# Performance work log

Hardware: AMD Instinct MI355X
Metric: run time of the kernel (lower is better)

The kernel has to match this reference:

```python
import jax, jax.numpy as jnp
import numpy as np

D_MODEL = 1024
N_HEADS = 16
HEAD_DIM = D_MODEL // N_HEADS
EPS = 1e-6


def _phi(x):
    # elu(x) + 1 feature map
    return jax.nn.elu(x) + 1.0


def setup_inputs() -> dict:
    key = jax.random.key(0)
    ks = jax.random.split(key, 12)
    B, N, M = 4, 4096, 4096
    s = 1.0 / np.sqrt(D_MODEL)
    return {
        "queries": jax.random.normal(ks[0], (B, N, D_MODEL), jnp.float32),
        "keys": jax.random.normal(ks[1], (B, M, D_MODEL), jnp.float32),
        "values": jax.random.normal(ks[2], (B, M, D_MODEL), jnp.float32),
        "wq": jax.random.normal(ks[3], (D_MODEL, D_MODEL), jnp.float32) * s,
        "bq": jax.random.normal(ks[4], (D_MODEL,), jnp.float32) * s,
        "wk": jax.random.normal(ks[5], (D_MODEL, D_MODEL), jnp.float32) * s,
        "bk": jax.random.normal(ks[6], (D_MODEL,), jnp.float32) * s,
        "wv": jax.random.normal(ks[7], (D_MODEL, D_MODEL), jnp.float32) * s,
        "bv": jax.random.normal(ks[8], (D_MODEL,), jnp.float32) * s,
        "wo": jax.random.normal(ks[9], (D_MODEL, D_MODEL), jnp.float32) * s,
        "bo": jax.random.normal(ks[10], (D_MODEL,), jnp.float32) * s,
    }


def reference(queries, keys, values, wq, bq, wk, bk, wv, bv, wo, bo):
    B, N, _ = queries.shape
    M = keys.shape[1]
    H, Dh = N_HEADS, HEAD_DIM
    # projections + head split -> [B, H, seq, Dh]
    q = _phi((queries @ wq.T + bq).reshape(B, N, H, Dh).transpose(0, 2, 1, 3))
    k = _phi((keys @ wk.T + bk).reshape(B, M, H, Dh).transpose(0, 2, 1, 3))
    v = (values @ wv.T + bv).reshape(B, M, H, Dh).transpose(0, 2, 1, 3)
    # kv aggregation: [B,H,Dh,Dh]
    kv = jnp.einsum("bhmd,bhme->bhde", k, v)
    # normalizer: [B,H,Dh]
    z = k.sum(axis=2)
    num = jnp.einsum("bhnd,bhde->bhne", q, kv)
    den = jnp.einsum("bhnd,bhd->bhn", q, z)[..., None] + EPS
    out = (num / den).transpose(0, 2, 1, 3).reshape(B, N, H * Dh)
    return out @ wo.T + bo
```

## Files before the change

kernel.cpp:

```cpp
#include <hip/hip_runtime.h>

#define EPS 1e-6f

typedef __attribute__((ext_vector_type(8))) __bf16 bf16x8;
typedef __attribute__((ext_vector_type(4))) float f32x4;
typedef __attribute__((ext_vector_type(4))) unsigned short us4v;
typedef __attribute__((ext_vector_type(8))) unsigned short us8v;
typedef unsigned short us;

__device__ inline us f2bf(float f) {
  unsigned int u = __builtin_bit_cast(unsigned int, f);
  unsigned int r = (u + 0x7fffu + ((u >> 16) & 1u)) >> 16;
  return (us)r;
}
__device__ inline float bf2f(us s) {
  unsigned int u = ((unsigned int)s) << 16;
  return __builtin_bit_cast(float, u);
}
__device__ inline unsigned int cvtpk(float a, float b) {
  unsigned int d;
  asm("v_cvt_pk_bf16_f32 %0, %1, %2" : "=v"(d) : "v"(a), "v"(b));
  return d;
}

__device__ inline void gl_lds16(const us* g, us* l) {
  __builtin_amdgcn_global_load_lds(
      (const __attribute__((address_space(1))) unsigned int*)g,
      (__attribute__((address_space(3))) unsigned int*)l, 16, 0, 0);
}

__global__ __launch_bounds__(256) void conv_w4(const float* __restrict__ wq,
                                               const float* __restrict__ wk,
                                               const float* __restrict__ wv,
                                               const float* __restrict__ wo,
                                               us* __restrict__ dq,
                                               us* __restrict__ dk,
                                               us* __restrict__ dv,
                                               us* __restrict__ dwo) {
  int bid = blockIdx.x;
  int msel = bid >> 9, lb = bid & 511;
  const float* s = (msel == 0) ? wq : (msel == 1) ? wk : (msel == 2) ? wv : wo;
  us* d = (msel == 0) ? dq : (msel == 1) ? dk : (msel == 2) ? dv : dwo;
  int idx = lb * 256 + threadIdx.x;
  size_t base = (size_t)idx * 8;
  float4 a = *(const float4*)(s + base);
  float4 b = *(const float4*)(s + base + 4);
  us8v o;
  o[0] = f2bf(a.x); o[1] = f2bf(a.y); o[2] = f2bf(a.z); o[3] = f2bf(a.w);
  o[4] = f2bf(b.x); o[5] = f2bf(b.y); o[6] = f2bf(b.z); o[7] = f2bf(b.w);
  *(us8v*)(d + base) = o;
}

template <int MODE>
__global__ __launch_bounds__(512, 2) void proj_gemm(const void* __restrict__ Xv,
                                                    const us* __restrict__ W,
                                                    const float* __restrict__ bias,
                                                    void* __restrict__ Yv) {
  constexpr bool FP32X = (MODE != 3);
  __shared__ alignas(16) us As[2][256 * 64];
  __shared__ alignas(16) us Bs[2][256 * 64];

  const float* Xf = (const float*)Xv;
  const us* Xh = (const us*)Xv;

  const int t = threadIdx.x;
  const int wave = t >> 6, lane = t & 63;
  const int q4 = lane >> 4, l16 = lane & 15;
  const int wm = wave >> 2, wn = wave & 3;
  const int bid = blockIdx.x;
  const int rowg = (bid & 7) * 8 + (bid >> 5);
  const int colg = (bid >> 3) & 3;
  const int rowBase = rowg << 8;
  const int colBase = colg << 8;

  const int tr = t >> 3;
  const int g8 = ((t & 7) ^ (tr & 7)) * 8;
  const us* Wg = W + (size_t)(colBase + tr) * 1024 + g8;

  const int gx0 = ((0 | q4) ^ (l16 & 7)) * 8;
  const int gx1 = ((4 | q4) ^ (l16 & 7)) * 8;
  const int arow_off = (wm * 128 + l16) * 64;
  const int brow_off = (wn * 64 + l16) * 64;

  float4 av[2][2][2];
  uint4 aw[2][2];

  f32x4 acc[8][4];
#pragma unroll
  for (int i = 0; i < 8; i++)
#pragma unroll
    for (int j = 0; j < 4; j++) acc[i][j] = (f32x4){0.f, 0.f, 0.f, 0.f};

#define ISSUE_A(kt, h)                                                       \
  if constexpr (FP32X) {                                                     \
    const float* p_ = Xf + (size_t)(rowBase + (h) * 128 + tr) * 1024 +       \
                      (kt) * 64 + g8;                                        \
    av[h][0][0] = *(const float4*)p_;                                        \
    av[h][0][1] = *(const float4*)(p_ + 4);                                  \
    av[h][1][0] = *(const float4*)(p_ + 65536);                              \
    av[h][1][1] = *(const float4*)(p_ + 65536 + 4);                          \
  } else {                                                                   \
    const us* p_ = Xh + (size_t)(rowBase + (h) * 128 + tr) * 1024 +          \
                   (kt) * 64 + g8;                                           \
    aw[h][0] = *(const uint4*)p_;                                            \
    aw[h][1] = *(const uint4*)(p_ + 65536);                                  \
  }

#define WRITE_A(kt, h)                                                       \
  _Pragma("unroll") for (int r_ = 0; r_ < 2; ++r_) {                         \
    uint4 o_;                                                                \
    if constexpr (FP32X) {                                                   \
      o_.x = cvtpk(av[h][r_][0].x, av[h][r_][0].y);                          \
      o_.y = cvtpk(av[h][r_][0].z, av[h][r_][0].w);                          \
      o_.z = cvtpk(av[h][r_][1].x, av[h][r_][1].y);                          \
      o_.w = cvtpk(av[h][r_][1].z, av[h][r_][1].w);                          \
    } else {                                                                 \
      o_ = aw[h][r_];                                                        \
    }                                                                        \
    *(uint4*)&As[(kt) & 1][((h) * 128 + wave * 8) * 64 + r_ * 4096 +         \
                           lane * 8] = o_;                                   \
  }

#define STAGE_B(kt, h)                                                       \
  {                                                                          \
    us* d_ = &Bs[(kt) & 1][((h) * 128 + wave * 8) * 64];                     \
    const us* s_ = Wg + (size_t)((h) * 128) * 1024 + (kt) * 64;              \
    gl_lds16(s_, d_);                                                        \
    gl_lds16(s_ + (size_t)64 * 1024, d_ + 64 * 64);                          \
  }
#define PH_SYNC_PRE()                                                        \
  asm volatile("s_barrier" ::: "memory");                                    \
  asm volatile("s_waitcnt lgkmcnt(0)" ::: "memory");                         \
  __builtin_amdgcn_sched_barrier(0);                                         \
  __builtin_amdgcn_s_setprio(1);
#define PH_SYNC_POST()                                                       \
  __builtin_amdgcn_s_setprio(0);                                            \
  asm volatile("s_barrier" ::: "memory");
#define MFMA16(J, AF)                                                        \
  _Pragma("unroll") for (int s_i = 0; s_i < 2; ++s_i)                        \
  _Pragma("unroll") for (int ks = 0; ks < 2; ++ks)                           \
  _Pragma("unroll") for (int ni = 0; ni < 4; ++ni)                           \
    acc[2 * (J) + s_i][ni] = __builtin_amdgcn_mfma_f32_16x16x32_bf16(        \
        AF[s_i][ks], bfv[ni][ks], acc[2 * (J) + s_i][ni], 0, 0, 0);

  STAGE_B(0, 0); STAGE_B(0, 1);
  ISSUE_A(0, 0); ISSUE_A(0, 1);
  STAGE_B(1, 0); STAGE_B(1, 1);
  asm volatile("s_waitcnt vmcnt(4)" ::: "memory");
  WRITE_A(0, 0); WRITE_A(0, 1);
  asm volatile("s_waitcnt lgkmcnt(0)" ::: "memory");
  asm volatile("s_barrier" ::: "memory");

#pragma unroll 2
  for (int m = 0; m < 16; ++m) {
    const int b = m & 1;
    const us* Ar = &As[b][arow_off];
    const us* Br = &Bs[b][brow_off];
    bf16x8 bfv[4][2];

    {
      bf16x8 af[2][2];
#pragma unroll
      for (int s_i = 0; s_i < 2; ++s_i) {
        af[s_i][0] = *(const bf16x8*)(Ar + (0 + s_i) * 1024 + gx0);
        af[s_i][1] = *(const bf16x8*)(Ar + (0 + s_i) * 1024 + gx1);
      }
#pragma unroll
      for (int ni = 0; ni < 4; ++ni) {
        bfv[ni][0] = *(const bf16x8*)(Br + ni * 1024 + gx0);
        bfv[ni][1] = *(const bf16x8*)(Br + ni * 1024 + gx1);
      }
      if (m < 15) { ISSUE_A(m + 1, 0); }
      PH_SYNC_PRE();
      MFMA16(0, af);
      PH_SYNC_POST();
    }
    {
      bf16x8 af[2][2];
#pragma unroll
      for (int s_i = 0; s_i < 2; ++s_i) {
        af[s_i][0] = *(const bf16x8*)(Ar + (2 + s_i) * 1024 + gx0);
        af[s_i][1] = *(const bf16x8*)(Ar + (2 + s_i) * 1024 + gx1);
      }
      if (m < 15) { ISSUE_A(m + 1, 1); }
      PH_SYNC_PRE();
      MFMA16(1, af);
      PH_SYNC_POST();
    }
    {
      bf16x8 af[2][2];
#pragma unroll
      for (int s_i = 0; s_i < 2; ++s_i) {
        af[s_i][0] = *(const bf16x8*)(Ar + (4 + s_i) * 1024 + gx0);
        af[s_i][1] = *(const bf16x8*)(Ar + (4 + s_i) * 1024 + gx1);
      }
      if (m < 15) {
        if constexpr (FP32X)
          asm volatile("s_waitcnt vmcnt(4)" ::: "memory");
        else
          asm volatile("s_waitcnt vmcnt(2)" ::: "memory");
        WRITE_A(m + 1, 0);
      }
      if (m < 14) STAGE_B(m + 2, 0);
      PH_SYNC_PRE();
      MFMA16(2, af);
      PH_SYNC_POST();
    }
    {
      bf16x8 af[2][2];
#pragma unroll
      for (int s_i = 0; s_i < 2; ++s_i) {
        af[s_i][0] = *(const bf16x8*)(Ar + (6 + s_i) * 1024 + gx0);
        af[s_i][1] = *(const bf16x8*)(Ar + (6 + s_i) * 1024 + gx1);
      }
      if (m < 15) {
        if (m < 14)
          asm volatile("s_waitcnt vmcnt(2)" ::: "memory");
        else
          asm volatile("s_waitcnt vmcnt(0)" ::: "memory");
        WRITE_A(m + 1, 1);
      }
      if (m < 14) STAGE_B(m + 2, 1);
      PH_SYNC_PRE();
      MFMA16(3, af);
      PH_SYNC_POST();
    }
  }
#undef ISSUE_A
#undef WRITE_A
#undef STAGE_B
#undef PH_SYNC_PRE
#undef PH_SYNC_POST
#undef MFMA16

#pragma unroll
  for (int j = 0; j < 4; j++) {
    int col = colBase + wn * 64 + j * 16 + l16;
    float bv = bias[col];
#pragma unroll
    for (int i = 0; i < 8; i++) {
      int row0 = rowBase + wm * 128 + i * 16 + q4 * 4;
      if (MODE == 1 || MODE == 2) {
        int bb = row0 >> 12, m0 = row0 & 4095;
        int h = col >> 6, dd = col & 63;
        us4v pk;
#pragma unroll
        for (int r = 0; r < 4; r++) {
          float y = acc[i][j][r] + bv;
          if (MODE == 1) y = (y > 0.f) ? (y + 1.f) : __expf(y);
          pk[r] = f2bf(y);
        }
        *(us4v*)&((us*)Yv)[(((size_t)((bb * 16 + h) * 64 + dd)) << 12) + m0] = pk;
      } else {
#pragma unroll
        for (int r = 0; r < 4; r++) {
          float y = acc[i][j][r] + bv;
          if (MODE == 0) {
            y = (y > 0.f) ? (y + 1.f) : __expf(y);
            ((us*)Yv)[(size_t)(row0 + r) * 1024 + col] = f2bf(y);
          } else {
            ((float*)Yv)[(size_t)(row0 + r) * 1024 + col] = y;
          }
        }
      }
    }
  }
}

__global__ __launch_bounds__(256) void kv_stage1(const us* __restrict__ kt,
                                                 const us* __restrict__ vt,
                                                 float* __restrict__ part,
                                                 float* __restrict__ zpart) {
  __shared__ float red[4][4096];
  __shared__ float zred[4][64][4];

  const int blk = blockIdx.x;
  const int bh = blk >> 2, split = blk & 3;
  const int t = threadIdx.x;
  const int w = t >> 6, lane = t & 63;
  const int q4 = lane >> 4, l16 = lane & 15;
  const us* ktb = kt + (size_t)bh * 64 * 4096;
  const us* vtb = vt + (size_t)bh * 64 * 4096;
  const int mbeg = split * 1024 + w * 256;

  f32x4 acc[4][4];
#pragma unroll
  for (int i = 0; i < 4; i++)
#pragma unroll
    for (int j = 0; j < 4; j++) acc[i][j] = (f32x4){0.f, 0.f, 0.f, 0.f};
  float zacc[4] = {0.f, 0.f, 0.f, 0.f};

  for (int m0 = mbeg; m0 < mbeg + 256; m0 += 32) {
    bf16x8 af[4], bfr[4];
#pragma unroll
    for (int i = 0; i < 4; i++)
      af[i] = *(const bf16x8*)&vtb[(size_t)(i * 16 + l16) * 4096 + m0 + q4 * 8];
#pragma unroll
    for (int j = 0; j < 4; j++) {
      us8v ub = *(const us8v*)&ktb[(size_t)(j * 16 + l16) * 4096 + m0 + q4 * 8];
      bfr[j] = __builtin_bit_cast(bf16x8, ub);
#pragma unroll
      for (int e = 0; e < 8; e++) zacc[j] += bf2f(ub[e]);
    }
#pragma unroll
    for (int i = 0; i < 4; i++)
#pragma unroll
      for (int j = 0; j < 4; j++)
        acc[i][j] = __builtin_amdgcn_mfma_f32_16x16x32_bf16(af[i], bfr[j], acc[i][j], 0, 0, 0);
  }

#pragma unroll
  for (int i = 0; i < 4; i++)
#pragma unroll
    for (int j = 0; j < 4; j++)
#pragma unroll
      for (int r = 0; r < 4; r++)
        red[w][(i * 16 + q4 * 4 + r) * 64 + j * 16 + l16] = acc[i][j][r];
#pragma unroll
  for (int j = 0; j < 4; j++) zred[w][j * 16 + l16][q4] = zacc[j];
  __syncthreads();

  float* pb = part + (size_t)blk * 4096;
#pragma unroll
  for (int i = 0; i < 16; i++) {
    int idx = t + 256 * i;
    pb[idx] = red[0][idx] + red[1][idx] + red[2][idx] + red[3][idx];
  }
  if (t < 64) {
    float s = 0.f;
#pragma unroll
    for (int w2 = 0; w2 < 4; w2++)
#pragma unroll
      for (int q = 0; q < 4; q++) s += zred[w2][t][q];
    zpart[blk * 64 + t] = s;
  }
}

__global__ __launch_bounds__(256) void kv_stage2(const float* __restrict__ part,
                                                 const float* __restrict__ zpart,
                                                 us* __restrict__ kvb,
                                                 float* __restrict__ z) {
  const int bh = blockIdx.x;
  const int t = threadIdx.x;
  const float* p0 = part + (size_t)bh * 4 * 4096;
#pragma unroll
  for (int i = 0; i < 16; i++) {
    int idx = t + 256 * i;
    float s = p0[idx] + p0[4096 + idx] + p0[8192 + idx] + p0[12288 + idx];
    kvb[(size_t)bh * 4096 + idx] = f2bf(s);
  }
  if (t < 64) {
    const float* zp = zpart + (size_t)bh * 4 * 64;
    z[bh * 64 + t] = zp[t] + zp[64 + t] + zp[128 + t] + zp[192 + t];
  }
}

__global__ __launch_bounds__(256) void attn_kernel(const us* __restrict__ q,
                                                   const us* __restrict__ kvb,
                                                   const float* __restrict__ z,
                                                   us* __restrict__ attn) {
  __shared__ alignas(16) us kvs[64 * 72];
  __shared__ float zs[64];
  __shared__ float invden[256];

  const int bid = blockIdx.x;
  const int bh = bid >> 4, nc = bid & 15;
  const int b = bh >> 4, h = bh & 15;
  const int n0 = nc * 256;
  const int t = threadIdx.x;
  const int wave = t >> 6, lane = t & 63;
  const int q4 = lane >> 4, l16 = lane & 15;

#pragma unroll
  for (int i = 0; i < 2; i++) {
    int chunk = t + 256 * i;
    int e = chunk >> 3, d8 = chunk & 7;
    us8v vv = *(const us8v*)&kvb[(size_t)bh * 4096 + chunk * 8];
    *(us8v*)&kvs[e * 72 + d8 * 8] = vv;
  }
  if (t < 64) zs[t] = z[bh * 64 + t];
  __syncthreads();

  {
    const us* qrow = q + ((size_t)(b * 4096 + n0 + t)) * 1024 + h * 64;
    float s = 0.f;
#pragma unroll
    for (int d0 = 0; d0 < 64; d0 += 8) {
      us8v v = *(const us8v*)(qrow + d0);
#pragma unroll
      for (int j = 0; j < 8; j++) s += bf2f(v[j]) * zs[d0 + j];
    }
    invden[t] = 1.0f / (s + EPS);
  }
  __syncthreads();

  f32x4 acc[4][4];
#pragma unroll
  for (int i = 0; i < 4; i++)
#pragma unroll
    for (int j = 0; j < 4; j++) acc[i][j] = (f32x4){0.f, 0.f, 0.f, 0.f};

  const us* qb = q + ((size_t)(b * 4096 + n0 + wave * 64)) * 1024 + h * 64;
#pragma unroll
  for (int ks = 0; ks < 2; ks++) {
    bf16x8 af[4], bfr[4];
#pragma unroll
    for (int i = 0; i < 4; i++)
      af[i] = *(const bf16x8*)(qb + (size_t)(i * 16 + l16) * 1024 + ks * 32 + q4 * 8);
#pragma unroll
    for (int j = 0; j < 4; j++)
      bfr[j] = *(const bf16x8*)&kvs[(j * 16 + l16) * 72 + ks * 32 + q4 * 8];
#pragma unroll
    for (int i = 0; i < 4; i++)
#pragma unroll
      for (int j = 0; j < 4; j++)
        acc[i][j] = __builtin_amdgcn_mfma_f32_16x16x32_bf16(af[i], bfr[j], acc[i][j], 0, 0, 0);
  }

  us* ab = attn + ((size_t)(b * 4096 + n0 + wave * 64)) * 1024 + h * 64;
#pragma unroll
  for (int i = 0; i < 4; i++)
#pragma unroll
    for (int j = 0; j < 4; j++)
#pragma unroll
      for (int r = 0; r < 4; r++) {
        int rowl = i * 16 + q4 * 4 + r;
        int nl = wave * 64 + rowl;
        int e = j * 16 + l16;
        ab[(size_t)rowl * 1024 + e] = f2bf(acc[i][j][r] * invden[nl]);
      }
}

extern "C" void kernel_launch(void* const* d_in, const int* in_sizes, int n_in,
                              void* d_out, int out_size, void* d_ws, size_t ws_size,
                              hipStream_t stream) {
  const float* queries = (const float*)d_in[0];
  const float* keys    = (const float*)d_in[1];
  const float* values  = (const float*)d_in[2];
  const float* wq = (const float*)d_in[3];
  const float* bq = (const float*)d_in[4];
  const float* wk = (const float*)d_in[5];
  const float* bk = (const float*)d_in[6];
  const float* wv = (const float*)d_in[7];
  const float* bv = (const float*)d_in[8];
  const float* wo = (const float*)d_in[9];
  const float* bo = (const float*)d_in[10];

  char* ws = (char*)d_ws;
  const size_t TB = (size_t)16384 * 1024 * 2;
  us* A   = (us*)(ws);
  us* Bb  = (us*)(ws + TB);
  us* wqb = (us*)(ws + 3 * TB);
  us* wkb = wqb + (size_t)1024 * 1024;
  us* wvb = wkb + (size_t)1024 * 1024;
  us* wob = wvb + (size_t)1024 * 1024;
  float* part  = (float*)(wob + (size_t)1024 * 1024);
  float* zpart = part + (size_t)256 * 4096;
  float* z     = zpart + 256 * 64;
  us* kvb      = (us*)(z + 4096);

  conv_w4<<<2048, 256, 0, stream>>>(wq, wk, wv, wo, wqb, wkb, wvb, wob);

  proj_gemm<1><<<256, 512, 0, stream>>>((const void*)keys, wkb, bk, (void*)A);
  proj_gemm<2><<<256, 512, 0, stream>>>((const void*)values, wvb, bv, (void*)Bb);
  kv_stage1<<<256, 256, 0, stream>>>(A, Bb, part, zpart);
  kv_stage2<<<64, 256, 0, stream>>>(part, zpart, kvb, z);
  proj_gemm<0><<<256, 512, 0, stream>>>((const void*)queries, wqb, bq, (void*)A);
  attn_kernel<<<1024, 256, 0, stream>>>(A, kvb, z, A);
  proj_gemm<3><<<256, 512, 0, stream>>>((const void*)A, wob, bo, d_out);
}
```

Measured before the change: 436.3 us.

## Deepen A-operand register prefetch to two k-tiles ahead in projection GEMM

The projection GEMM now double-buffers the A-tile register staging, issuing global loads two k-steps ahead instead of one. The main loop is rewritten as explicit paired windows with hand-set vmcnt waits, plus special-cased tail windows. The aim is to hide more global-load latency behind the MFMA phases. In exchange it doubles the staging registers (notably the fp32 path's float4 buffers), which could lower occupancy or cause spills, and it depends on carefully tuned wait counts.

```diff
diff --git a/kernel.cpp b/kernel.cpp
--- a/kernel.cpp
+++ b/kernel.cpp
@@ -28,6 +28,9 @@
       (const __attribute__((address_space(1))) unsigned int*)g,
       (__attribute__((address_space(3))) unsigned int*)l, 16, 0, 0);
 }
+
+#define STR_(x) #x
+#define WAITV(n) asm volatile("s_waitcnt vmcnt(" STR_(n) ")" ::: "memory")
 
 __global__ __launch_bounds__(256) void conv_w4(const float* __restrict__ wq,
                                                const float* __restrict__ wk,
@@ -82,8 +85,8 @@
   const int arow_off = (wm * 128 + l16) * 64;
   const int brow_off = (wn * 64 + l16) * 64;
 
-  float4 av[2][2][2];
-  uint4 aw[2][2];
+  float4 avb[2][2][2][2];
+  uint4 awb[2][2][2];
 
   f32x4 acc[8][4];
 #pragma unroll
@@ -91,31 +94,31 @@
 #pragma unroll
     for (int j = 0; j < 4; j++) acc[i][j] = (f32x4){0.f, 0.f, 0.f, 0.f};
 
-#define ISSUE_A(kt, h)                                                       \
+#define ISSUE_A(BUF, kt, h)                                                  \
   if constexpr (FP32X) {                                                     \
     const float* p_ = Xf + (size_t)(rowBase + (h) * 128 + tr) * 1024 +       \
                       (kt) * 64 + g8;                                        \
-    av[h][0][0] = *(const float4*)p_;                                        \
-    av[h][0][1] = *(const float4*)(p_ + 4);                                  \
-    av[h][1][0] = *(const float4*)(p_ + 65536);                              \
-    av[h][1][1] = *(const float4*)(p_ + 65536 + 4);                          \
+    avb[BUF][h][0][0] = *(const float4*)p_;                                  \
+    avb[BUF][h][0][1] = *(const float4*)(p_ + 4);                            \
+    avb[BUF][h][1][0] = *(const float4*)(p_ + 65536);                        \
+    avb[BUF][h][1][1] = *(const float4*)(p_ + 65536 + 4);                    \
   } else {                                                                   \
     const us* p_ = Xh + (size_t)(rowBase + (h) * 128 + tr) * 1024 +          \
                    (kt) * 64 + g8;                                           \
-    aw[h][0] = *(const uint4*)p_;                                            \
-    aw[h][1] = *(const uint4*)(p_ + 65536);                                  \
-  }
-
-#define WRITE_A(kt, h)                                                       \
+    awb[BUF][h][0] = *(const uint4*)p_;                                      \
+    awb[BUF][h][1] = *(const uint4*)(p_ + 65536);                            \
+  }
+
+#define WRITE_A(BUF, kt, h)                                                  \
   _Pragma("unroll") for (int r_ = 0; r_ < 2; ++r_) {                         \
     uint4 o_;                                                                \
     if constexpr (FP32X) {                                                   \
-      o_.x = cvtpk(av[h][r_][0].x, av[h][r_][0].y);                          \
-      o_.y = cvtpk(av[h][r_][0].z, av[h][r_][0].w);                          \
-      o_.z = cvtpk(av[h][r_][1].x, av[h][r_][1].y);                          \
-      o_.w = cvtpk(av[h][r_][1].z, av[h][r_][1].w);                          \
+      o_.x = cvtpk(avb[BUF][h][r_][0].x, avb[BUF][h][r_][0].y);              \
+      o_.y = cvtpk(avb[BUF][h][r_][0].z, avb[BUF][h][r_][0].w);              \
+      o_.z = cvtpk(avb[BUF][h][r_][1].x, avb[BUF][h][r_][1].y);              \
+      o_.w = cvtpk(avb[BUF][h][r_][1].z, avb[BUF][h][r_][1].w);              \
     } else {                                                                 \
-      o_ = aw[h][r_];                                                        \
+      o_ = awb[BUF][h][r_];                                                  \
     }                                                                        \
     *(uint4*)&As[(kt) & 1][((h) * 128 + wave * 8) * 64 + r_ * 4096 +         \
                            lane * 8] = o_;                                   \
@@ -127,6 +130,11 @@
     const us* s_ = Wg + (size_t)((h) * 128) * 1024 + (kt) * 64;              \
     gl_lds16(s_, d_);                                                        \
     gl_lds16(s_ + (size_t)64 * 1024, d_ + 64 * 64);                          \
+  }
+#define RD_A(af, base)                                                       \
+  _Pragma("unroll") for (int s_i = 0; s_i < 2; ++s_i) {                      \
+    af[s_i][0] = *(const bf16x8*)(Ar + ((base) + s_i) * 1024 + gx0);         \
+    af[s_i][1] = *(const bf16x8*)(Ar + ((base) + s_i) * 1024 + gx1);         \
   }
 #define PH_SYNC_PRE()                                                        \
   asm volatile("s_barrier" ::: "memory");                                    \
@@ -143,92 +151,88 @@
     acc[2 * (J) + s_i][ni] = __builtin_amdgcn_mfma_f32_16x16x32_bf16(        \
         AF[s_i][ks], bfv[ni][ks], acc[2 * (J) + s_i][ni], 0, 0, 0);
 
+#define WINDOW(m, CUR, NXT, ISSA, WRA, STGB, V1, V2, V3)                     \
+  {                                                                          \
+    const us* Ar = &As[(m) & 1][arow_off];                                   \
+    const us* Br = &Bs[(m) & 1][brow_off];                                   \
+    bf16x8 bfv[4][2];                                                        \
+    {                            \
+      bf16x8 af[2][2];                                                       \
+      RD_A(af, 0);                                                           \
+      _Pragma("unroll") for (int ni = 0; ni < 4; ++ni) {                     \
+        bfv[ni][0] = *(const bf16x8*)(Br + ni * 1024 + gx0);                 \
+        bfv[ni][1] = *(const bf16x8*)(Br + ni * 1024 + gx1);                 \
+      }                                                                      \
+      if (ISSA) { ISSUE_A(NXT, (m) + 2, 0); }                                \
+      PH_SYNC_PRE(); MFMA16(0, af); PH_SYNC_POST();                          \
+    }                                                                        \
+    {                                    \
+      bf16x8 af[2][2];                                                       \
+      RD_A(af, 2);                                                           \
+      if (ISSA) { ISSUE_A(NXT, (m) + 2, 1); }                                \
+      PH_SYNC_PRE(); MFMA16(1, af); PH_SYNC_POST();                          \
+    }                                                                        \
+    {            \
+      bf16x8 af[2][2];                                                       \
+      RD_A(af, 4);                                                           \
+      if (WRA) { WAITV(V1); WRITE_A(CUR, (m) + 1, 0); }                      \
+      if (STGB) STAGE_B((m) + 2, 0);                                         \
+      PH_SYNC_PRE(); MFMA16(2, af); PH_SYNC_POST();                          \
+    }                                                                        \
+    {  \
+      bf16x8 af[2][2];                                                       \
+      RD_A(af, 6);                                                           \
+      if (WRA) { WAITV(V2); WRITE_A(CUR, (m) + 1, 1); }                      \
+      if (STGB) STAGE_B((m) + 2, 1);                                         \
+      asm volatile("s_barrier" ::: "memory");                                \
+      asm volatile("s_waitcnt lgkmcnt(0)" ::: "memory");                     \
+      __builtin_amdgcn_sched_barrier(0);                                     \
+      __builtin_amdgcn_s_setprio(1);                                         \
+      MFMA16(3, af);                                                         \
+      __builtin_amdgcn_s_setprio(0);                                         \
+      WAITV(V3);                                                             \
+      asm volatile("s_barrier" ::: "memory");                                \
+    }                                                                        \
+  }
+
+  ISSUE_A(0, 0, 0); ISSUE_A(0, 0, 1);
   STAGE_B(0, 0); STAGE_B(0, 1);
-  ISSUE_A(0, 0); ISSUE_A(0, 1);
+  ISSUE_A(1, 1, 0); ISSUE_A(1, 1, 1);
   STAGE_B(1, 0); STAGE_B(1, 1);
-  asm volatile("s_waitcnt vmcnt(4)" ::: "memory");
-  WRITE_A(0, 0); WRITE_A(0, 1);
+  if constexpr (FP32X) {
+    WAITV(16);
+    WRITE_A(0, 0, 0); WRITE_A(0, 0, 1);
+    WAITV(12);
+  } else {
+    WAITV(12);
+    WRITE_A(0, 0, 0); WRITE_A(0, 0, 1);
+    WAITV(8);
+  }
   asm volatile("s_waitcnt lgkmcnt(0)" ::: "memory");
   asm volatile("s_barrier" ::: "memory");
 
-#pragma unroll 2
-  for (int m = 0; m < 16; ++m) {
-    const int b = m & 1;
-    const us* Ar = &As[b][arow_off];
-    const us* Br = &Bs[b][brow_off];
-    bf16x8 bfv[4][2];
-
-    {
-      bf16x8 af[2][2];
-#pragma unroll
-      for (int s_i = 0; s_i < 2; ++s_i) {
-        af[s_i][0] = *(const bf16x8*)(Ar + (0 + s_i) * 1024 + gx0);
-        af[s_i][1] = *(const bf16x8*)(Ar + (0 + s_i) * 1024 + gx1);
-      }
-#pragma unroll
-      for (int ni = 0; ni < 4; ++ni) {
-        bfv[ni][0] = *(const bf16x8*)(Br + ni * 1024 + gx0);
-        bfv[ni][1] = *(const bf16x8*)(Br + ni * 1024 + gx1);
-      }
-      if (m < 15) { ISSUE_A(m + 1, 0); }
-      PH_SYNC_PRE();
-      MFMA16(0, af);
-      PH_SYNC_POST();
+  if constexpr (FP32X) {
+    for (int mb = 0; mb < 7; ++mb) {
+      const int m = 2 * mb;
+      WINDOW(m, 1, 0, 1, 1, 1, 16, 14, 12);
+      WINDOW(m + 1, 0, 1, 1, 1, 1, 16, 14, 12);
     }
-    {
-      bf16x8 af[2][2];
-#pragma unroll
-      for (int s_i = 0; s_i < 2; ++s_i) {
-        af[s_i][0] = *(const bf16x8*)(Ar + (2 + s_i) * 1024 + gx0);
-        af[s_i][1] = *(const bf16x8*)(Ar + (2 + s_i) * 1024 + gx1);
-      }
-      if (m < 15) { ISSUE_A(m + 1, 1); }
-      PH_SYNC_PRE();
-      MFMA16(1, af);
-      PH_SYNC_POST();
+    WINDOW(14, 1, 0, 0, 1, 0, 8, 4, 0);
+    WINDOW(15, 0, 1, 0, 0, 0, 0, 0, 0);
+  } else {
+    for (int mb = 0; mb < 7; ++mb) {
+      const int m = 2 * mb;
+      WINDOW(m, 1, 0, 1, 1, 1, 10, 10, 8);
+      WINDOW(m + 1, 0, 1, 1, 1, 1, 10, 10, 8);
     }
-    {
-      bf16x8 af[2][2];
-#pragma unroll
-      for (int s_i = 0; s_i < 2; ++s_i) {
-        af[s_i][0] = *(const bf16x8*)(Ar + (4 + s_i) * 1024 + gx0);
-        af[s_i][1] = *(const bf16x8*)(Ar + (4 + s_i) * 1024 + gx1);
-      }
-      if (m < 15) {
-        if constexpr (FP32X)
-          asm volatile("s_waitcnt vmcnt(4)" ::: "memory");
-        else
-          asm volatile("s_waitcnt vmcnt(2)" ::: "memory");
-        WRITE_A(m + 1, 0);
-      }
-      if (m < 14) STAGE_B(m + 2, 0);
-      PH_SYNC_PRE();
-      MFMA16(2, af);
-      PH_SYNC_POST();
-    }
-    {
-      bf16x8 af[2][2];
-#pragma unroll
-      for (int s_i = 0; s_i < 2; ++s_i) {
-        af[s_i][0] = *(const bf16x8*)(Ar + (6 + s_i) * 1024 + gx0);
-        af[s_i][1] = *(const bf16x8*)(Ar + (6 + s_i) * 1024 + gx1);
-      }
-      if (m < 15) {
-        if (m < 14)
-          asm volatile("s_waitcnt vmcnt(2)" ::: "memory");
-        else
-          asm volatile("s_waitcnt vmcnt(0)" ::: "memory");
-        WRITE_A(m + 1, 1);
-      }
-      if (m < 14) STAGE_B(m + 2, 1);
-      PH_SYNC_PRE();
-      MFMA16(3, af);
-      PH_SYNC_POST();
-    }
-  }
+    WINDOW(14, 1, 0, 0, 1, 0, 6, 4, 0);
+    WINDOW(15, 0, 1, 0, 0, 0, 0, 0, 0);
+  }
+#undef WINDOW
 #undef ISSUE_A
 #undef WRITE_A
 #undef STAGE_B
+#undef RD_A
 #undef PH_SYNC_PRE
 #undef PH_SYNC_POST
 #undef MFMA16
```

Result: no change. 444.0 us (+1.8%).
